# Performance work log

Hardware: AMD Instinct MI355X
Metric: run time of the kernel (lower is better)

## Reference

```python
import jax, jax.numpy as jnp
import numpy as np
from jax import lax

B, S, F, H, O, U = 512, 168, 12, 128, 3, 256
PERIODS = (3, 6, 12, 24)


def _glorot(key, shape):
    fan_in = shape[-1]
    fan_out = shape[-2] if len(shape) >= 2 else shape[-1]
    scale = jnp.sqrt(2.0 / (fan_in + fan_out))
    return jax.random.normal(key, shape, jnp.float32) * scale


def setup_inputs() -> dict:
    key = jax.random.key(0)
    ks = iter(jax.random.split(key, 64))
    inp = {"x": jax.random.normal(next(ks), (B, 1, F, S), jnp.float32)}
    # 3 SFF groups (group1: enc_in=12, groups 2/3: enc_in=3) share conv/linear shapes per period
    for p in PERIODS:
        k = 1 + 2 * (p // 2)
        inp[f"conv{p}"] = _glorot(next(ks), (3, k))             # [group, kernel]
        inp[f"lin{p}"] = _glorot(next(ks), (3, S // p, S // p))  # [group, seg_y, seg_x]
    inp["Wb0"] = _glorot(next(ks), (U, F + H)); inp["bb0"] = jnp.zeros((U,), jnp.float32)
    inp["Wb1"] = _glorot(next(ks), (U, U));     inp["bb1"] = jnp.zeros((U,), jnp.float32)
    inp["Wff1"] = _glorot(next(ks), (H, U));    inp["bff1"] = jnp.zeros((H,), jnp.float32)
    inp["Wff2"] = _glorot(next(ks), (H, U));    inp["bff2"] = jnp.zeros((H,), jnp.float32)
    inp["Wta"] = _glorot(next(ks), (H, U));     inp["bta"] = jnp.zeros((H,), jnp.float32)
    inp["Wtb"] = _glorot(next(ks), (H, U));     inp["btb"] = jnp.zeros((H,), jnp.float32)
    inp["Wfc"] = _glorot(next(ks), (O, H));     inp["bfc"] = jnp.zeros((O,), jnp.float32)
    inp["Wfits"] = _glorot(next(ks), (O, S, S))  # FF: individual per-channel linear seq->pred
    return inp


def _sff(x, conv_w, lin_w, p):
    # x: [B, S, C]; conv_w: [k]; lin_w: [seg_y, seg_x]
    Bx, Sx, C = x.shape
    xp = jnp.transpose(x, (0, 2, 1))                      # [B, C, S]
    xr = xp.reshape(Bx * C, 1, Sx)
    pad = p // 2
    conv = lax.conv_general_dilated(xr, conv_w.reshape(1, 1, -1), (1,), [(pad, pad)],
                                    dimension_numbers=("NCH", "OIH", "NCH"))
    xc = conv.reshape(Bx, C, Sx) + xp                     # residual smoothing
    seg = Sx // p
    xc = jnp.transpose(xc.reshape(Bx * C, seg, p), (0, 2, 1))  # [B*C, p, seg_x]
    y = jnp.einsum("npk,qk->npq", xc, lin_w)              # [B*C, p, seg_y]
    y = jnp.transpose(y, (0, 2, 1)).reshape(Bx, C, -1)    # [B, C, pred]
    return jnp.transpose(y, (0, 2, 1))                    # [B, pred, C]


def reference(x, conv3, lin3, conv6, lin6, conv12, lin12, conv24, lin24,
              Wb0, bb0, Wb1, bb1, Wff1, bff1, Wff2, bff2,
              Wta, bta, Wtb, btb, Wfc, bfc, Wfits):
    convs = {3: conv3, 6: conv6, 12: conv12, 24: conv24}
    lins = {3: lin3, 6: lin6, 12: lin12, 24: lin24}

    xs = jnp.transpose(x[:, 0], (0, 2, 1))                # [B, S, F]
    seq_mean = jnp.mean(xs, axis=1, keepdims=True)        # [B, 1, F]
    xs = xs - seq_mean

    x1 = sum(_sff(xs, convs[p][0], lins[p][0], p) for p in PERIODS) * 0.25   # [B,S,F]
    xin3 = x1[:, :, :3]
    x2 = sum(_sff(xin3, convs[p][1], lins[p][1], p) for p in PERIODS) * 0.25  # [B,S,3]
    x3 = sum(_sff(xin3, convs[p][2], lins[p][2], p) for p in PERIODS) * 0.25  # [B,S,3]

    # CfC recurrence (ts == 1.0 everywhere; dropout in eval mode = identity)
    def step(h, xt):
        z = jnp.concatenate([xt, h], axis=1)
        z = jax.nn.silu(z @ Wb0.T + bb0)
        z = jax.nn.silu(z @ Wb1.T + bb1)
        ff1 = jnp.tanh(z @ Wff1.T + bff1)
        ff2 = jnp.tanh(z @ Wff2.T + bff2)
        t_interp = jax.nn.sigmoid((z @ Wta.T + bta) + (z @ Wtb.T + btb))
        h_new = ff1 * (1.0 - t_interp) + t_interp * ff2
        return h_new, h_new

    h0 = jnp.zeros((x1.shape[0], Wff1.shape[0]), x1.dtype)
    _, hs = lax.scan(step, h0, jnp.transpose(x1, (1, 0, 2)))  # hs: [S, B, H]

    readout = jnp.einsum("sbh,oh->bso", hs, Wfc) + bfc        # [B, S, O]
    readout = readout + x3
    readout = jnp.einsum("bsc,cps->bpc", readout, Wfits)      # FF (per-channel S -> pred)
    return readout + seq_mean[:, :, :3] + x2
```

## Files before the change

kernel.cpp:

```cpp
#include <hip/hip_runtime.h>

#define BB 512
#define SS 168
#define FF 12
#define HH 128
#define UU 256

typedef unsigned short u16;
typedef unsigned int   u32;
typedef _Float16 f16x8 __attribute__((ext_vector_type(8)));
typedef float    f32x4 __attribute__((ext_vector_type(4)));

__device__ __forceinline__ float sigmoidf_(float x){ return __fdividef(1.f, 1.f + __expf(-x)); }
__device__ __forceinline__ float siluf_(float x){ return x * sigmoidf_(x); }
__device__ __forceinline__ float tanhf_(float x){
    float t = __expf(-2.f * fabsf(x));
    float y = __fdividef(1.f - t, 1.f + t);
    return copysignf(y, x);
}
__device__ __forceinline__ u16 f2h_(float v){ return __builtin_bit_cast(u16, (_Float16)v); }
__device__ __forceinline__ f16x8 bc8_(uint4 v){ return __builtin_bit_cast(f16x8, v); }
__device__ __forceinline__ int aslot_(int row, int k){
    return (k >> 5) * 512 + ((k & 31) >> 3) * 128 + row * 8 + (k & 7);
}

#define MFMA16(a, b, acc) __builtin_amdgcn_mfma_f32_16x16x32_f16((a), (b), (acc), 0, 0, 0)

#define PREP_BLOCKS 810
#define SFFA_BLOCKS (BB * FF)

__global__ __launch_bounds__(256) void front_kernel(
    const float* __restrict__ x,
    const float* __restrict__ c3,  const float* __restrict__ l3,
    const float* __restrict__ c6,  const float* __restrict__ l6,
    const float* __restrict__ c12, const float* __restrict__ l12,
    const float* __restrict__ c24, const float* __restrict__ l24,
    const float* __restrict__ Wb0, const float* __restrict__ Wb1,
    const float* __restrict__ Wff1, const float* __restrict__ Wff2,
    const float* __restrict__ Wta, const float* __restrict__ Wtb,
    const float* __restrict__ Wfc,
    u16* __restrict__ W0f, u16* __restrict__ W1f, u16* __restrict__ W4f,
    float* __restrict__ meanbuf, float* __restrict__ x1,
    float* __restrict__ x2, float* __restrict__ x3)
{
    if (blockIdx.x < PREP_BLOCKS) {
        int t = blockIdx.x * 256 + threadIdx.x;
        if (t < 43520) {
            int e = t & 7, c = (t >> 3) & 15, g = (t >> 7) & 3, rest = t >> 9;
            int s = rest % 5, tt = rest / 5;
            int k = s * 32 + g * 8 + e;
            float v;
            if (tt < 16) { int u = tt * 16 + c; v = (k < 140) ? Wb0[u * 140 + k] : 0.f; }
            else         { v = (c < 3 && k >= 12 && k < 140) ? Wfc[c * 128 + (k - 12)] : 0.f; }
            W0f[t] = f2h_(v);
        } else if (t < 43520 + 65536) {
            int t1 = t - 43520;
            int e = t1 & 7, c = (t1 >> 3) & 15, g = (t1 >> 7) & 3, rest = t1 >> 9;
            int s = rest & 7, tt = rest >> 3;
            int u = tt * 16 + c, k = s * 32 + g * 8 + e;
            W1f[t1] = f2h_(Wb1[u * 256 + k]);
        } else if (t < 43520 + 65536 + 98304) {
            int t2 = t - 109056;
            int e = t2 & 7, c = (t2 >> 3) & 15, g = (t2 >> 7) & 3, rest = t2 >> 9;
            int s = rest & 7, tt = rest >> 3;
            int u = (tt & 7) * 16 + c, k = s * 32 + g * 8 + e;
            float v;
            if      (tt < 8)  v = Wff1[u * 256 + k];
            else if (tt < 16) v = Wff2[u * 256 + k];
            else              v = Wta[u * 256 + k] + Wtb[u * 256 + k];
            W4f[t2] = f2h_(v);
        }
        return;
    }

    int bc = blockIdx.x - PREP_BLOCKS;
    int b = bc / FF, c = bc % FF;
    __shared__ float v[SS], cv[SS], red[256];
    int tid = threadIdx.x;

    float raw = 0.f;
    if (tid < SS) raw = x[(b * FF + c) * SS + tid];
    red[tid] = raw;
    __syncthreads();
    for (int off = 128; off > 0; off >>= 1) {
        if (tid < off) red[tid] += red[tid + off];
        __syncthreads();
    }
    float mv = red[0] * (1.f / SS);
    if (tid == 0) meanbuf[b * FF + c] = mv;
    if (tid < SS) v[tid] = raw - mv;
    __syncthreads();

    const float* cw[4]  = {c3, c6, c12, c24};
    const float* lwv[4] = {l3, l6, l12, l24};
    const int P[4] = {3, 6, 12, 24};
    float acc = 0.f;
    for (int pi = 0; pi < 4; ++pi) {
        int p = P[pi], pad = p >> 1, k = 1 + 2 * pad, seg = SS / p;
        const float* cwp = cw[pi];
        float cc = 0.f;
        if (tid < SS) {
            cc = v[tid];
            for (int j = 0; j < k; ++j) {
                int t = tid + j - pad;
                if (t >= 0 && t < SS) cc += cwp[j] * v[t];
            }
        }
        __syncthreads();
        if (tid < SS) cv[tid] = cc;
        __syncthreads();
        if (tid < SS) {
            int q = tid / p, ph = tid - q * p;
            const float* lwp = lwv[pi];
            float a = 0.f;
            for (int kk = 0; kk < seg; ++kk) a += lwp[q * seg + kk] * cv[kk * p + ph];
            acc += a;
        }
    }
    float x1v = 0.25f * acc;
    if (tid < SS) x1[(b * SS + tid) * FF + c] = x1v;
    if (c >= 3) return;

    __syncthreads();
    if (tid < SS) v[tid] = x1v;
    __syncthreads();
    float acc2 = 0.f, acc3 = 0.f;
    for (int pi = 0; pi < 4; ++pi) {
        int p = P[pi], pad = p >> 1, k = 1 + 2 * pad, seg = SS / p;
        for (int row = 1; row <= 2; ++row) {
            const float* cwp = cw[pi] + row * k;
            float cc = 0.f;
            if (tid < SS) {
                cc = v[tid];
                for (int j = 0; j < k; ++j) {
                    int t = tid + j - pad;
                    if (t >= 0 && t < SS) cc += cwp[j] * v[t];
                }
            }
            __syncthreads();
            if (tid < SS) cv[tid] = cc;
            __syncthreads();
            if (tid < SS) {
                int q = tid / p, ph = tid - q * p;
                const float* lwp = lwv[pi] + row * seg * seg;
                float a = 0.f;
                for (int kk = 0; kk < seg; ++kk) a += lwp[q * seg + kk] * cv[kk * p + ph];
                if (row == 1) acc2 += a; else acc3 += a;
            }
        }
    }
    if (tid < SS) {
        x2[(b * SS + tid) * 3 + c] = 0.25f * acc2;
        x3[(b * SS + tid) * 3 + c] = 0.25f * acc3;
    }
}

__global__ __launch_bounds__(512, 2) void scan_kernel(
    const float* __restrict__ x1g,
    const uint4* __restrict__ W0f, const uint4* __restrict__ W1f, const uint4* __restrict__ W4f,
    const float* __restrict__ bb0, const float* __restrict__ bb1,
    const float* __restrict__ bff1, const float* __restrict__ bff2,
    const float* __restrict__ bta,  const float* __restrict__ btb,
    const float* __restrict__ bfc,
    float* __restrict__ r1g)
{
    const int b0 = blockIdx.x * 4;
    const int tid = threadIdx.x;
    const int w = tid >> 6, lane = tid & 63;
    const int cl = lane & 15, grp = lane >> 4;

    __shared__ __align__(16) u16 W0ro_s[2560];
    __shared__ __align__(16) u16 xh[8064];
    __shared__ __align__(16) u16 zin_s[2560];
    __shared__ __align__(16) u16 z1_s[4096];
    __shared__ __align__(16) u16 z2_s[4096];
    __shared__ __align__(16) float r1s[2016];
    __shared__ float bfcs[4];

    uint4* W0ro4 = (uint4*)W0ro_s;
    uint4* zin4  = (uint4*)zin_s;
    uint4* z1_4  = (uint4*)z1_s;
    uint4* z2_4  = (uint4*)z2_s;

    f16x8 w0a[5], w0b[5];
    f16x8 w1f0[8], w1f1[8], w4a[8], w4b[8], w4c[8];
    #pragma unroll
    for (int s = 0; s < 5; ++s) {
        w0a[s] = bc8_(W0f[((w    ) * 5 + s) * 64 + lane]);
        w0b[s] = bc8_(W0f[((w + 8) * 5 + s) * 64 + lane]);
    }
    #pragma unroll
    for (int s = 0; s < 8; ++s) {
        w1f0[s] = bc8_(W1f[((w     ) * 8 + s) * 64 + lane]);
        w1f1[s] = bc8_(W1f[((w +  8) * 8 + s) * 64 + lane]);
        w4a[s]  = bc8_(W4f[((w     ) * 8 + s) * 64 + lane]);
        w4b[s]  = bc8_(W4f[((w +  8) * 8 + s) * 64 + lane]);
        w4c[s]  = bc8_(W4f[((w + 16) * 8 + s) * 64 + lane]);
    }
    const int u = w * 16 + cl;
    const float bz1a = bb0[u],  bz1b = bb0[128 + u];
    const float bz2a = bb1[u],  bz2b = bb1[128 + u];
    const float bf1r = bff1[u], bf2r = bff2[u];
    const float btsr = bta[u] + btb[u];

    for (int i = tid; i < 320; i += 512) W0ro4[i] = W0f[5120 + i];
    for (int i = tid; i < 8064; i += 512) {
        int s = i / 48, rem = i - s * 48, r = rem / 12, ii = rem - r * 12;
        xh[i] = f2h_(x1g[((b0 + r) * SS + s) * FF + ii]);
    }
    for (int i = tid; i < 320; i += 512) zin4[i] = make_uint4(0, 0, 0, 0);
    for (int i = tid; i < 512; i += 512) z1_4[i] = make_uint4(0, 0, 0, 0);
    for (int i = tid; i < 512; i += 512) z2_4[i] = make_uint4(0, 0, 0, 0);
    if (tid < 3) bfcs[tid] = bfc[tid];
    __syncthreads();
    if (tid < 48) {
        int r = tid / 12, i = tid % 12;
        zin_s[aslot_(r * 4, i)] = xh[tid];
    }
    __syncthreads();

    #pragma unroll 1
    for (int s = 0; s < SS; ++s) {
        f32x4 a1a0 = {0.f,0.f,0.f,0.f}, a1a1 = {0.f,0.f,0.f,0.f};
        f32x4 a1b0 = {0.f,0.f,0.f,0.f}, a1b1 = {0.f,0.f,0.f,0.f};
        f32x4 accr = {0.f,0.f,0.f,0.f};
        #pragma unroll
        for (int ks = 0; ks < 5; ++ks) {
            f16x8 av = bc8_(zin4[ks * 64 + lane]);
            if (ks & 1) { a1a1 = MFMA16(av, w0a[ks], a1a1); a1b1 = MFMA16(av, w0b[ks], a1b1); }
            else        { a1a0 = MFMA16(av, w0a[ks], a1a0); a1b0 = MFMA16(av, w0b[ks], a1b0); }
            if (w == 0) accr = MFMA16(av, bc8_(W0ro4[ks * 64 + lane]), accr);
        }
        if (w == 0 && s > 0 && cl < 3)
            r1s[grp * 504 + (s - 1) * 3 + cl] = accr[0] + bfcs[cl];

        {
            int tr = grp * 4;
            z1_s[aslot_(tr, u)]       = f2h_(siluf_(a1a0[0] + a1a1[0] + bz1a));
            z1_s[aslot_(tr, 128 + u)] = f2h_(siluf_(a1b0[0] + a1b1[0] + bz1b));
        }
        __syncthreads();

        f32x4 a2a0 = {0.f,0.f,0.f,0.f}, a2a1 = {0.f,0.f,0.f,0.f};
        f32x4 a2b0 = {0.f,0.f,0.f,0.f}, a2b1 = {0.f,0.f,0.f,0.f};
        #pragma unroll
        for (int ks = 0; ks < 8; ++ks) {
            f16x8 av = bc8_(z1_4[ks * 64 + lane]);
            if (ks & 1) { a2a1 = MFMA16(av, w1f0[ks], a2a1); a2b1 = MFMA16(av, w1f1[ks], a2b1); }
            else        { a2a0 = MFMA16(av, w1f0[ks], a2a0); a2b0 = MFMA16(av, w1f1[ks], a2b0); }
        }
        {
            int tr = grp * 4;
            z2_s[aslot_(tr, u)]       = f2h_(siluf_(a2a0[0] + a2a1[0] + bz2a));
            z2_s[aslot_(tr, 128 + u)] = f2h_(siluf_(a2b0[0] + a2b1[0] + bz2b));
        }
        __syncthreads();

        f32x4 c3a0 = {0.f,0.f,0.f,0.f}, c3a1 = {0.f,0.f,0.f,0.f};
        f32x4 c3b0 = {0.f,0.f,0.f,0.f}, c3b1 = {0.f,0.f,0.f,0.f};
        f32x4 c3c0 = {0.f,0.f,0.f,0.f}, c3c1 = {0.f,0.f,0.f,0.f};
        #pragma unroll
        for (int ks = 0; ks < 8; ++ks) {
            f16x8 av = bc8_(z2_4[ks * 64 + lane]);
            if (ks & 1) {
                c3a1 = MFMA16(av, w4a[ks], c3a1);
                c3b1 = MFMA16(av, w4b[ks], c3b1);
                c3c1 = MFMA16(av, w4c[ks], c3c1);
            } else {
                c3a0 = MFMA16(av, w4a[ks], c3a0);
                c3b0 = MFMA16(av, w4b[ks], c3b0);
                c3c0 = MFMA16(av, w4c[ks], c3c0);
            }
        }

        {
            float ff1v = tanhf_(c3a0[0] + c3a1[0] + bf1r);
            float ff2v = tanhf_(c3b0[0] + c3b1[0] + bf2r);
            float tv   = sigmoidf_(c3c0[0] + c3c1[0] + btsr);
            float h    = ff1v + tv * (ff2v - ff1v);
            zin_s[aslot_(grp * 4, 12 + u)] = f2h_(h);
        }
        if (tid >= 448 && tid < 496 && s + 1 < SS) {
            int idx = tid - 448;
            int r = idx / 12, i = idx % 12;
            zin_s[aslot_(r * 4, i)] = xh[(s + 1) * 48 + idx];
        }
        __syncthreads();
    }

    if (w == 0) {
        f32x4 accr = {0.f, 0.f, 0.f, 0.f};
        #pragma unroll
        for (int ks = 0; ks < 5; ++ks)
            accr = MFMA16(bc8_(zin4[ks * 64 + lane]),
                          bc8_(W0ro4[ks * 64 + lane]), accr);
        if (cl < 3)
            r1s[grp * 504 + 167 * 3 + cl] = accr[0] + bfcs[cl];
    }
    __syncthreads();
    for (int idx = tid; idx < 2016; idx += 512) {
        int r = idx / 504, rem = idx - r * 504;
        r1g[(b0 + r) * 504 + rem] = r1s[r * 504 + rem];
    }
}

__global__ __launch_bounds__(256) void fits_kernel(
    const float* __restrict__ r1, const float* __restrict__ x3,
    const float* __restrict__ Wfits,
    const float* __restrict__ x2, const float* __restrict__ meanbuf,
    float* __restrict__ out)
{
    int bid = blockIdx.x;
    int bt = bid & 7;
    int rest = bid >> 3;
    int c = rest % 3;
    int pt = rest / 3;
    int b0 = bt * 64, p0 = pt * 28;
    __shared__ float rT[168][65];
    __shared__ float wT[28][168];
    int t = threadIdx.x;
    for (int idx = t; idx < 64 * 168; idx += 256) {
        int b = idx / 168, s = idx - b * 168;
        int gi = ((b0 + b) * 168 + s) * 3 + c;
        rT[s][b] = r1[gi] + x3[gi];
    }
    for (int idx = t; idx < 28 * 168; idx += 256) {
        int p = idx / 168, s = idx - p * 168;
        wT[p][s] = Wfits[(c * 168 + p0 + p) * 168 + s];
    }
    __syncthreads();
    int b = t & 63, pq = t >> 6;
    float acc[7] = {0, 0, 0, 0, 0, 0, 0};
    for (int s = 0; s < 168; ++s) {
        float v = rT[s][b];
        #pragma unroll
        for (int j = 0; j < 7; ++j) acc[j] += v * wT[pq * 7 + j][s];
    }
    float mb = meanbuf[(b0 + b) * 12 + c];
    #pragma unroll
    for (int j = 0; j < 7; ++j) {
        int p = p0 + pq * 7 + j;
        int gi = ((b0 + b) * 168 + p) * 3 + c;
        out[gi] = acc[j] + mb + x2[gi];
    }
}

extern "C" void kernel_launch(void* const* d_in, const int* in_sizes, int n_in,
                              void* d_out, int out_size, void* d_ws, size_t ws_size,
                              hipStream_t stream) {
    const float* x    = (const float*)d_in[0];
    const float* c3   = (const float*)d_in[1];
    const float* l3   = (const float*)d_in[2];
    const float* c6   = (const float*)d_in[3];
    const float* l6   = (const float*)d_in[4];
    const float* c12  = (const float*)d_in[5];
    const float* l12  = (const float*)d_in[6];
    const float* c24  = (const float*)d_in[7];
    const float* l24  = (const float*)d_in[8];
    const float* Wb0  = (const float*)d_in[9];
    const float* bb0  = (const float*)d_in[10];
    const float* Wb1  = (const float*)d_in[11];
    const float* bb1  = (const float*)d_in[12];
    const float* Wff1 = (const float*)d_in[13];
    const float* bff1 = (const float*)d_in[14];
    const float* Wff2 = (const float*)d_in[15];
    const float* bff2 = (const float*)d_in[16];
    const float* Wta  = (const float*)d_in[17];
    const float* bta  = (const float*)d_in[18];
    const float* Wtb  = (const float*)d_in[19];
    const float* btb  = (const float*)d_in[20];
    const float* Wfc  = (const float*)d_in[21];
    const float* bfc  = (const float*)d_in[22];
    const float* Wfits= (const float*)d_in[23];

    float* ws      = (float*)d_ws;
    float* meanbuf = ws;
    float* x1      = meanbuf + 6144;
    float* x2      = x1 + 1032192;
    float* x3      = x2 + 258048;
    float* r1      = x3 + 258048;
    u16*   W0f     = (u16*)(r1 + 258048);
    u16*   W1f     = W0f + 43520;
    u16*   W4f     = W1f + 65536;
    float* out     = (float*)d_out;

    front_kernel<<<PREP_BLOCKS + SFFA_BLOCKS, 256, 0, stream>>>(
        x, c3, l3, c6, l6, c12, l12, c24, l24,
        Wb0, Wb1, Wff1, Wff2, Wta, Wtb, Wfc,
        W0f, W1f, W4f, meanbuf, x1, x2, x3);
    scan_kernel<<<BB / 4, 512, 0, stream>>>(x1,
                                            (const uint4*)W0f, (const uint4*)W1f, (const uint4*)W4f,
                                            bb0, bb1, bff1, bff2, bta, btb, bfc, r1);
    fits_kernel<<<144, 256, 0, stream>>>(r1, x3, Wfits, x2, meanbuf, out);
}
```

Measured before the change: 342.2 us.

## Fuse SFF front end, CfC scan and FF readout into one kernel

Merges the three launches into a single per-4-batch kernel. Each block computes the mean, SFF smoothing, the scan, and the Wfits projection in shared memory, and loads fp32 weights directly into fp16 MFMA fragments, so there is no separate weight-prep pass and no global round-trips for x1/x2/x3/r1. The 12-wide input projection moves out of the MFMA into scalar FMAs precomputed one step ahead, the K loop drops from 5 to 4, biases are folded into accumulator init, and s_setprio is added around the MFMA blocks. The cost is that every block now does redundant weight conversion and serial SFF/readout work on only 128 blocks, with heavy LDS use.

```diff
diff --git a/kernel.cpp b/kernel.cpp
--- a/kernel.cpp
+++ b/kernel.cpp
@@ -7,7 +7,6 @@
 #define UU 256
 
 typedef unsigned short u16;
-typedef unsigned int   u32;
 typedef _Float16 f16x8 __attribute__((ext_vector_type(8)));
 typedef float    f32x4 __attribute__((ext_vector_type(4)));
 
@@ -23,242 +22,264 @@
 __device__ __forceinline__ int aslot_(int row, int k){
     return (k >> 5) * 512 + ((k & 31) >> 3) * 128 + row * 8 + (k & 7);
 }
+__device__ __forceinline__ f16x8 pack8_(const float* p){
+    float4 a = *(const float4*)p, b = *(const float4*)(p + 4);
+    f16x8 r;
+    r[0]=(_Float16)a.x; r[1]=(_Float16)a.y; r[2]=(_Float16)a.z; r[3]=(_Float16)a.w;
+    r[4]=(_Float16)b.x; r[5]=(_Float16)b.y; r[6]=(_Float16)b.z; r[7]=(_Float16)b.w;
+    return r;
+}
+__device__ __forceinline__ f16x8 pack8sum_(const float* p, const float* q){
+    float4 a = *(const float4*)p, b = *(const float4*)(p + 4);
+    float4 c = *(const float4*)q, d = *(const float4*)(q + 4);
+    f16x8 r;
+    r[0]=(_Float16)(a.x+c.x); r[1]=(_Float16)(a.y+c.y); r[2]=(_Float16)(a.z+c.z); r[3]=(_Float16)(a.w+c.w);
+    r[4]=(_Float16)(b.x+d.x); r[5]=(_Float16)(b.y+d.y); r[6]=(_Float16)(b.z+d.z); r[7]=(_Float16)(b.w+d.w);
+    return r;
+}
 
 #define MFMA16(a, b, acc) __builtin_amdgcn_mfma_f32_16x16x32_f16((a), (b), (acc), 0, 0, 0)
 
-#define PREP_BLOCKS 810
-#define SFFA_BLOCKS (BB * FF)
-
-__global__ __launch_bounds__(256) void front_kernel(
-    const float* __restrict__ x,
-    const float* __restrict__ c3,  const float* __restrict__ l3,
-    const float* __restrict__ c6,  const float* __restrict__ l6,
-    const float* __restrict__ c12, const float* __restrict__ l12,
-    const float* __restrict__ c24, const float* __restrict__ l24,
-    const float* __restrict__ Wb0, const float* __restrict__ Wb1,
-    const float* __restrict__ Wff1, const float* __restrict__ Wff2,
-    const float* __restrict__ Wta, const float* __restrict__ Wtb,
-    const float* __restrict__ Wfc,
-    u16* __restrict__ W0f, u16* __restrict__ W1f, u16* __restrict__ W4f,
-    float* __restrict__ meanbuf, float* __restrict__ x1,
-    float* __restrict__ x2, float* __restrict__ x3)
-{
-    if (blockIdx.x < PREP_BLOCKS) {
-        int t = blockIdx.x * 256 + threadIdx.x;
-        if (t < 43520) {
-            int e = t & 7, c = (t >> 3) & 15, g = (t >> 7) & 3, rest = t >> 9;
-            int s = rest % 5, tt = rest / 5;
-            int k = s * 32 + g * 8 + e;
-            float v;
-            if (tt < 16) { int u = tt * 16 + c; v = (k < 140) ? Wb0[u * 140 + k] : 0.f; }
-            else         { v = (c < 3 && k >= 12 && k < 140) ? Wfc[c * 128 + (k - 12)] : 0.f; }
-            W0f[t] = f2h_(v);
-        } else if (t < 43520 + 65536) {
-            int t1 = t - 43520;
-            int e = t1 & 7, c = (t1 >> 3) & 15, g = (t1 >> 7) & 3, rest = t1 >> 9;
-            int s = rest & 7, tt = rest >> 3;
-            int u = tt * 16 + c, k = s * 32 + g * 8 + e;
-            W1f[t1] = f2h_(Wb1[u * 256 + k]);
-        } else if (t < 43520 + 65536 + 98304) {
-            int t2 = t - 109056;
-            int e = t2 & 7, c = (t2 >> 3) & 15, g = (t2 >> 7) & 3, rest = t2 >> 9;
-            int s = rest & 7, tt = rest >> 3;
-            int u = (tt & 7) * 16 + c, k = s * 32 + g * 8 + e;
-            float v;
-            if      (tt < 8)  v = Wff1[u * 256 + k];
-            else if (tt < 16) v = Wff2[u * 256 + k];
-            else              v = Wta[u * 256 + k] + Wtb[u * 256 + k];
-            W4f[t2] = f2h_(v);
-        }
-        return;
-    }
-
-    int bc = blockIdx.x - PREP_BLOCKS;
-    int b = bc / FF, c = bc % FF;
-    __shared__ float v[SS], cv[SS], red[256];
-    int tid = threadIdx.x;
-
-    float raw = 0.f;
-    if (tid < SS) raw = x[(b * FF + c) * SS + tid];
-    red[tid] = raw;
-    __syncthreads();
-    for (int off = 128; off > 0; off >>= 1) {
-        if (tid < off) red[tid] += red[tid + off];
-        __syncthreads();
-    }
-    float mv = red[0] * (1.f / SS);
-    if (tid == 0) meanbuf[b * FF + c] = mv;
-    if (tid < SS) v[tid] = raw - mv;
-    __syncthreads();
-
-    const float* cw[4]  = {c3, c6, c12, c24};
-    const float* lwv[4] = {l3, l6, l12, l24};
-    const int P[4] = {3, 6, 12, 24};
-    float acc = 0.f;
-    for (int pi = 0; pi < 4; ++pi) {
-        int p = P[pi], pad = p >> 1, k = 1 + 2 * pad, seg = SS / p;
-        const float* cwp = cw[pi];
-        float cc = 0.f;
-        if (tid < SS) {
-            cc = v[tid];
-            for (int j = 0; j < k; ++j) {
-                int t = tid + j - pad;
-                if (t >= 0 && t < SS) cc += cwp[j] * v[t];
-            }
-        }
-        __syncthreads();
-        if (tid < SS) cv[tid] = cc;
-        __syncthreads();
-        if (tid < SS) {
-            int q = tid / p, ph = tid - q * p;
-            const float* lwp = lwv[pi];
-            float a = 0.f;
-            for (int kk = 0; kk < seg; ++kk) a += lwp[q * seg + kk] * cv[kk * p + ph];
-            acc += a;
-        }
-    }
-    float x1v = 0.25f * acc;
-    if (tid < SS) x1[(b * SS + tid) * FF + c] = x1v;
-    if (c >= 3) return;
-
-    __syncthreads();
-    if (tid < SS) v[tid] = x1v;
-    __syncthreads();
-    float acc2 = 0.f, acc3 = 0.f;
-    for (int pi = 0; pi < 4; ++pi) {
-        int p = P[pi], pad = p >> 1, k = 1 + 2 * pad, seg = SS / p;
-        for (int row = 1; row <= 2; ++row) {
-            const float* cwp = cw[pi] + row * k;
-            float cc = 0.f;
-            if (tid < SS) {
-                cc = v[tid];
-                for (int j = 0; j < k; ++j) {
-                    int t = tid + j - pad;
-                    if (t >= 0 && t < SS) cc += cwp[j] * v[t];
-                }
-            }
-            __syncthreads();
-            if (tid < SS) cv[tid] = cc;
-            __syncthreads();
-            if (tid < SS) {
-                int q = tid / p, ph = tid - q * p;
-                const float* lwp = lwv[pi] + row * seg * seg;
-                float a = 0.f;
-                for (int kk = 0; kk < seg; ++kk) a += lwp[q * seg + kk] * cv[kk * p + ph];
-                if (row == 1) acc2 += a; else acc3 += a;
-            }
-        }
-    }
-    if (tid < SS) {
-        x2[(b * SS + tid) * 3 + c] = 0.25f * acc2;
-        x3[(b * SS + tid) * 3 + c] = 0.25f * acc3;
-    }
-}
-
-__global__ __launch_bounds__(512, 2) void scan_kernel(
-    const float* __restrict__ x1g,
-    const uint4* __restrict__ W0f, const uint4* __restrict__ W1f, const uint4* __restrict__ W4f,
-    const float* __restrict__ bb0, const float* __restrict__ bb1,
-    const float* __restrict__ bff1, const float* __restrict__ bff2,
-    const float* __restrict__ bta,  const float* __restrict__ btb,
-    const float* __restrict__ bfc,
-    float* __restrict__ r1g)
+__global__ __launch_bounds__(512, 2) void fused_kernel(
+    const float* __restrict__ xg,
+    const float* __restrict__ c3w,  const float* __restrict__ l3w,
+    const float* __restrict__ c6w,  const float* __restrict__ l6w,
+    const float* __restrict__ c12w, const float* __restrict__ l12w,
+    const float* __restrict__ c24w, const float* __restrict__ l24w,
+    const float* __restrict__ Wb0,  const float* __restrict__ bb0,
+    const float* __restrict__ Wb1,  const float* __restrict__ bb1,
+    const float* __restrict__ Wff1, const float* __restrict__ bff1,
+    const float* __restrict__ Wff2, const float* __restrict__ bff2,
+    const float* __restrict__ Wta,  const float* __restrict__ bta,
+    const float* __restrict__ Wtb,  const float* __restrict__ btb,
+    const float* __restrict__ Wfc,  const float* __restrict__ bfc,
+    const float* __restrict__ Wfits,
+    float* __restrict__ outg)
 {
     const int b0 = blockIdx.x * 4;
     const int tid = threadIdx.x;
     const int w = tid >> 6, lane = tid & 63;
     const int cl = lane & 15, grp = lane >> 4;
 
-    __shared__ __align__(16) u16 W0ro_s[2560];
-    __shared__ __align__(16) u16 xh[8064];
-    __shared__ __align__(16) u16 zin_s[2560];
-    __shared__ __align__(16) u16 z1_s[4096];
-    __shared__ __align__(16) u16 z2_s[4096];
-    __shared__ __align__(16) float r1s[2016];
+    __shared__ __align__(16) float xf[8064];
+    __shared__ __align__(16) float xraw[8064];
+    __shared__ __align__(16) float cvbuf[8064];
+    __shared__ __align__(16) float aux[6048];
+    __shared__ float meanloc[48];
     __shared__ float bfcs[4];
 
-    uint4* W0ro4 = (uint4*)W0ro_s;
+    u16* zin_s  = (u16*)xraw;
+    u16* z1_s   = ((u16*)xraw) + 2048;
+    u16* z2_s   = ((u16*)xraw) + 6144;
+    u16* W0ro_s = ((u16*)xraw) + 10240;
     uint4* zin4  = (uint4*)zin_s;
     uint4* z1_4  = (uint4*)z1_s;
     uint4* z2_4  = (uint4*)z2_s;
-
-    f16x8 w0a[5], w0b[5];
-    f16x8 w1f0[8], w1f1[8], w4a[8], w4b[8], w4c[8];
+    uint4* W0ro4 = (uint4*)W0ro_s;
+    float* r1s   = aux;
+    float* x2loc = aux + 2016;
+    float* x3loc = aux + 4032;
+
+    for (int i = tid; i < 8064; i += 512) {
+        int r = i / 2016, rem = i - r * 2016;
+        xraw[i] = xg[(b0 + r) * 2016 + rem];
+    }
+    if (tid < 3) bfcs[tid] = bfc[tid];
+    __syncthreads();
+
+    if (w < 6) {
+        int sidx = w * 8 + (lane >> 3), j = lane & 7;
+        float sum = 0.f;
+        for (int t = j; t < SS; t += 8) sum += xraw[sidx * 168 + t];
+        sum += __shfl_xor(sum, 1); sum += __shfl_xor(sum, 2); sum += __shfl_xor(sum, 4);
+        if (j == 0) meanloc[sidx] = sum * (1.f / 168.f);
+    }
+    __syncthreads();
+    for (int i = tid; i < 8064; i += 512) xraw[i] -= meanloc[i / 168];
+    __syncthreads();
+
+    const float* cws[4] = {c3w, c6w, c12w, c24w};
+    const float* lws[4] = {l3w, l6w, l12w, l24w};
+    const int    Pp[4]  = {3, 6, 12, 24};
+
+    float accA[16];
     #pragma unroll
-    for (int s = 0; s < 5; ++s) {
-        w0a[s] = bc8_(W0f[((w    ) * 5 + s) * 64 + lane]);
-        w0b[s] = bc8_(W0f[((w + 8) * 5 + s) * 64 + lane]);
-    }
+    for (int ii = 0; ii < 16; ++ii) accA[ii] = 0.f;
+    for (int pi = 0; pi < 4; ++pi) {
+        int p = Pp[pi], pad = p >> 1, kk_ = 1 + 2 * pad, seg = SS / p;
+        const float* cwp = cws[pi];
+        #pragma unroll 1
+        for (int ii = 0; ii < 16; ++ii) {
+            int i = tid + ii * 512;
+            if (i < 8064) {
+                int sr = i / 168, t = i - sr * 168;
+                const float* vs = &xraw[sr * 168];
+                float cc = vs[t];
+                for (int j = 0; j < kk_; ++j) {
+                    int tt = t + j - pad;
+                    if (tt >= 0 && tt < SS) cc += cwp[j] * vs[tt];
+                }
+                cvbuf[i] = cc;
+            }
+        }
+        __syncthreads();
+        const float* lwp = lws[pi];
+        #pragma unroll 1
+        for (int ii = 0; ii < 16; ++ii) {
+            int i = tid + ii * 512;
+            if (i < 8064) {
+                int sr = i / 168, t = i - sr * 168;
+                int q = t / p, ph = t - q * p;
+                const float* cvs = &cvbuf[sr * 168];
+                float a = 0.f;
+                for (int kk = 0; kk < seg; ++kk) a += lwp[q * seg + kk] * cvs[kk * p + ph];
+                accA[ii] += a;
+            }
+        }
+        __syncthreads();
+    }
+    #pragma unroll 1
+    for (int ii = 0; ii < 16; ++ii) {
+        int i = tid + ii * 512;
+        if (i < 8064) {
+            int sr = i / 168, t = i - sr * 168;
+            int r = sr / 12, c = sr - r * 12;
+            xf[r * 2016 + t * 12 + c] = 0.25f * accA[ii];
+        }
+    }
+    __syncthreads();
+
+    for (int i = tid; i < 256; i += 512) zin4[i] = make_uint4(0, 0, 0, 0);
+    for (int i = tid; i < 2048; i += 512) {
+        int ks = i >> 9, rem = i & 511;
+        int g = rem >> 7, c = (rem >> 3) & 15, e = rem & 7;
+        int k = ks * 32 + g * 8 + e;
+        W0ro_s[i] = f2h_((c < 3) ? Wfc[c * 128 + k] : 0.f);
+    }
+
+    float acc2[4], acc3[4];
     #pragma unroll
-    for (int s = 0; s < 8; ++s) {
-        w1f0[s] = bc8_(W1f[((w     ) * 8 + s) * 64 + lane]);
-        w1f1[s] = bc8_(W1f[((w +  8) * 8 + s) * 64 + lane]);
-        w4a[s]  = bc8_(W4f[((w     ) * 8 + s) * 64 + lane]);
-        w4b[s]  = bc8_(W4f[((w +  8) * 8 + s) * 64 + lane]);
-        w4c[s]  = bc8_(W4f[((w + 16) * 8 + s) * 64 + lane]);
-    }
+    for (int ii = 0; ii < 4; ++ii) { acc2[ii] = 0.f; acc3[ii] = 0.f; }
+    for (int pi = 0; pi < 4; ++pi) {
+        int p = Pp[pi], pad = p >> 1, kk_ = 1 + 2 * pad, seg = SS / p;
+        for (int row = 1; row <= 2; ++row) {
+            const float* cwp = cws[pi] + row * kk_;
+            #pragma unroll 1
+            for (int ii = 0; ii < 4; ++ii) {
+                int i = tid + ii * 512;
+                if (i < 2016) {
+                    int sr = i / 168, t = i - sr * 168;
+                    int r = sr / 3, c = sr - (sr / 3) * 3;
+                    float cc = xf[r * 2016 + t * 12 + c];
+                    for (int j = 0; j < kk_; ++j) {
+                        int tt = t + j - pad;
+                        if (tt >= 0 && tt < SS) cc += cwp[j] * xf[r * 2016 + tt * 12 + c];
+                    }
+                    cvbuf[i] = cc;
+                }
+            }
+            __syncthreads();
+            const float* lwp = lws[pi] + row * seg * seg;
+            #pragma unroll 1
+            for (int ii = 0; ii < 4; ++ii) {
+                int i = tid + ii * 512;
+                if (i < 2016) {
+                    int sr = i / 168, t = i - sr * 168;
+                    int q = t / p, ph = t - q * p;
+                    float a = 0.f;
+                    for (int kk = 0; kk < seg; ++kk) a += lwp[q * seg + kk] * cvbuf[sr * 168 + kk * p + ph];
+                    if (row == 1) acc2[ii] += a; else acc3[ii] += a;
+                }
+            }
+            __syncthreads();
+        }
+    }
+    #pragma unroll 1
+    for (int ii = 0; ii < 4; ++ii) {
+        int i = tid + ii * 512;
+        if (i < 2016) {
+            int sr = i / 168, t = i - sr * 168;
+            int r = sr / 3, c = sr - (sr / 3) * 3;
+            x2loc[r * 504 + t * 3 + c] = 0.25f * acc2[ii];
+            x3loc[r * 504 + t * 3 + c] = 0.25f * acc3[ii];
+        }
+    }
+
     const int u = w * 16 + cl;
+    f16x8 w0a[4], w0b[4], w1f0[8], w1f1[8], w4a[8], w4b[8], w4c[8];
+    #pragma unroll
+    for (int s8 = 0; s8 < 4; ++s8) {
+        int k0 = s8 * 32 + grp * 8;
+        w0a[s8] = pack8_(&Wb0[u * 140 + 12 + k0]);
+        w0b[s8] = pack8_(&Wb0[(128 + u) * 140 + 12 + k0]);
+    }
+    #pragma unroll
+    for (int s8 = 0; s8 < 8; ++s8) {
+        int k0 = s8 * 32 + grp * 8;
+        w1f0[s8] = pack8_(&Wb1[u * 256 + k0]);
+        w1f1[s8] = pack8_(&Wb1[(128 + u) * 256 + k0]);
+        w4a[s8]  = pack8_(&Wff1[u * 256 + k0]);
+        w4b[s8]  = pack8_(&Wff2[u * 256 + k0]);
+        w4c[s8]  = pack8sum_(&Wta[u * 256 + k0], &Wtb[u * 256 + k0]);
+    }
+    float w0xa[12], w0xb[12];
+    {
+        const float* pa = &Wb0[u * 140];
+        const float* pb = &Wb0[(128 + u) * 140];
+        #pragma unroll
+        for (int i = 0; i < 12; ++i) { w0xa[i] = pa[i]; w0xb[i] = pb[i]; }
+    }
     const float bz1a = bb0[u],  bz1b = bb0[128 + u];
     const float bz2a = bb1[u],  bz2b = bb1[128 + u];
     const float bf1r = bff1[u], bf2r = bff2[u];
     const float btsr = bta[u] + btb[u];
-
-    for (int i = tid; i < 320; i += 512) W0ro4[i] = W0f[5120 + i];
-    for (int i = tid; i < 8064; i += 512) {
-        int s = i / 48, rem = i - s * 48, r = rem / 12, ii = rem - r * 12;
-        xh[i] = f2h_(x1g[((b0 + r) * SS + s) * FF + ii]);
-    }
-    for (int i = tid; i < 320; i += 512) zin4[i] = make_uint4(0, 0, 0, 0);
-    for (int i = tid; i < 512; i += 512) z1_4[i] = make_uint4(0, 0, 0, 0);
-    for (int i = tid; i < 512; i += 512) z2_4[i] = make_uint4(0, 0, 0, 0);
-    if (tid < 3) bfcs[tid] = bfc[tid];
-    __syncthreads();
-    if (tid < 48) {
-        int r = tid / 12, i = tid % 12;
-        zin_s[aslot_(r * 4, i)] = xh[tid];
-    }
-    __syncthreads();
+    __syncthreads();
+
+    float z1xa = 0.f, z1xb = 0.f;
+    {
+        const float* xrow = &xf[grp * 2016];
+        #pragma unroll
+        for (int i = 0; i < 12; ++i) { float xv = xrow[i]; z1xa += w0xa[i] * xv; z1xb += w0xb[i] * xv; }
+    }
 
     #pragma unroll 1
     for (int s = 0; s < SS; ++s) {
-        f32x4 a1a0 = {0.f,0.f,0.f,0.f}, a1a1 = {0.f,0.f,0.f,0.f};
-        f32x4 a1b0 = {0.f,0.f,0.f,0.f}, a1b1 = {0.f,0.f,0.f,0.f};
-        f32x4 accr = {0.f,0.f,0.f,0.f};
-        #pragma unroll
-        for (int ks = 0; ks < 5; ++ks) {
+        f32x4 a1a0 = {z1xa + bz1a, 0.f, 0.f, 0.f}, a1a1 = {0.f, 0.f, 0.f, 0.f};
+        f32x4 a1b0 = {z1xb + bz1b, 0.f, 0.f, 0.f}, a1b1 = {0.f, 0.f, 0.f, 0.f};
+        f32x4 accr = {0.f, 0.f, 0.f, 0.f};
+        __builtin_amdgcn_s_setprio(1);
+        #pragma unroll
+        for (int ks = 0; ks < 4; ++ks) {
             f16x8 av = bc8_(zin4[ks * 64 + lane]);
             if (ks & 1) { a1a1 = MFMA16(av, w0a[ks], a1a1); a1b1 = MFMA16(av, w0b[ks], a1b1); }
             else        { a1a0 = MFMA16(av, w0a[ks], a1a0); a1b0 = MFMA16(av, w0b[ks], a1b0); }
             if (w == 0) accr = MFMA16(av, bc8_(W0ro4[ks * 64 + lane]), accr);
         }
+        __builtin_amdgcn_s_setprio(0);
         if (w == 0 && s > 0 && cl < 3)
             r1s[grp * 504 + (s - 1) * 3 + cl] = accr[0] + bfcs[cl];
-
-        {
-            int tr = grp * 4;
-            z1_s[aslot_(tr, u)]       = f2h_(siluf_(a1a0[0] + a1a1[0] + bz1a));
-            z1_s[aslot_(tr, 128 + u)] = f2h_(siluf_(a1b0[0] + a1b1[0] + bz1b));
-        }
-        __syncthreads();
-
-        f32x4 a2a0 = {0.f,0.f,0.f,0.f}, a2a1 = {0.f,0.f,0.f,0.f};
-        f32x4 a2b0 = {0.f,0.f,0.f,0.f}, a2b1 = {0.f,0.f,0.f,0.f};
+        z1_s[aslot_(grp * 4, u)]       = f2h_(siluf_(a1a0[0] + a1a1[0]));
+        z1_s[aslot_(grp * 4, 128 + u)] = f2h_(siluf_(a1b0[0] + a1b1[0]));
+        __syncthreads();
+
+        f32x4 a2a0 = {bz2a, 0.f, 0.f, 0.f}, a2a1 = {0.f, 0.f, 0.f, 0.f};
+        f32x4 a2b0 = {bz2b, 0.f, 0.f, 0.f}, a2b1 = {0.f, 0.f, 0.f, 0.f};
+        __builtin_amdgcn_s_setprio(1);
         #pragma unroll
         for (int ks = 0; ks < 8; ++ks) {
             f16x8 av = bc8_(z1_4[ks * 64 + lane]);
             if (ks & 1) { a2a1 = MFMA16(av, w1f0[ks], a2a1); a2b1 = MFMA16(av, w1f1[ks], a2b1); }
             else        { a2a0 = MFMA16(av, w1f0[ks], a2a0); a2b0 = MFMA16(av, w1f1[ks], a2b0); }
         }
-        {
-            int tr = grp * 4;
-            z2_s[aslot_(tr, u)]       = f2h_(siluf_(a2a0[0] + a2a1[0] + bz2a));
-            z2_s[aslot_(tr, 128 + u)] = f2h_(siluf_(a2b0[0] + a2b1[0] + bz2b));
-        }
-        __syncthreads();
-
-        f32x4 c3a0 = {0.f,0.f,0.f,0.f}, c3a1 = {0.f,0.f,0.f,0.f};
-        f32x4 c3b0 = {0.f,0.f,0.f,0.f}, c3b1 = {0.f,0.f,0.f,0.f};
-        f32x4 c3c0 = {0.f,0.f,0.f,0.f}, c3c1 = {0.f,0.f,0.f,0.f};
+        __builtin_amdgcn_s_setprio(0);
+        z2_s[aslot_(grp * 4, u)]       = f2h_(siluf_(a2a0[0] + a2a1[0]));
+        z2_s[aslot_(grp * 4, 128 + u)] = f2h_(siluf_(a2b0[0] + a2b1[0]));
+        __syncthreads();
+
+        f32x4 c3a0 = {bf1r, 0.f, 0.f, 0.f}, c3a1 = {0.f, 0.f, 0.f, 0.f};
+        f32x4 c3b0 = {bf2r, 0.f, 0.f, 0.f}, c3b1 = {0.f, 0.f, 0.f, 0.f};
+        f32x4 c3c0 = {btsr, 0.f, 0.f, 0.f}, c3c1 = {0.f, 0.f, 0.f, 0.f};
+        __builtin_amdgcn_s_setprio(1);
         #pragma unroll
         for (int ks = 0; ks < 8; ++ks) {
             f16x8 av = bc8_(z2_4[ks * 64 + lane]);
@@ -272,18 +293,23 @@
                 c3c0 = MFMA16(av, w4c[ks], c3c0);
             }
         }
+        __builtin_amdgcn_s_setprio(0);
 
         {
-            float ff1v = tanhf_(c3a0[0] + c3a1[0] + bf1r);
-            float ff2v = tanhf_(c3b0[0] + c3b1[0] + bf2r);
-            float tv   = sigmoidf_(c3c0[0] + c3c1[0] + btsr);
+            int sn = (s + 1 < SS) ? s + 1 : s;
+            const float* xrow = &xf[grp * 2016 + sn * 12];
+            float za = 0.f, zb = 0.f;
+            #pragma unroll
+            for (int i = 0; i < 12; ++i) { float xv = xrow[i]; za += w0xa[i] * xv; zb += w0xb[i] * xv; }
+            z1xa = za; z1xb = zb;
+        }
+
+        {
+            float ff1v = tanhf_(c3a0[0] + c3a1[0]);
+            float ff2v = tanhf_(c3b0[0] + c3b1[0]);
+            float tv   = sigmoidf_(c3c0[0] + c3c1[0]);
             float h    = ff1v + tv * (ff2v - ff1v);
-            zin_s[aslot_(grp * 4, 12 + u)] = f2h_(h);
-        }
-        if (tid >= 448 && tid < 496 && s + 1 < SS) {
-            int idx = tid - 448;
-            int r = idx / 12, i = idx % 12;
-            zin_s[aslot_(r * 4, i)] = xh[(s + 1) * 48 + idx];
+            zin_s[aslot_(grp * 4, u)] = f2h_(h);
         }
         __syncthreads();
     }
@@ -291,57 +317,33 @@
     if (w == 0) {
         f32x4 accr = {0.f, 0.f, 0.f, 0.f};
         #pragma unroll
-        for (int ks = 0; ks < 5; ++ks)
-            accr = MFMA16(bc8_(zin4[ks * 64 + lane]),
-                          bc8_(W0ro4[ks * 64 + lane]), accr);
-        if (cl < 3)
-            r1s[grp * 504 + 167 * 3 + cl] = accr[0] + bfcs[cl];
-    }
-    __syncthreads();
-    for (int idx = tid; idx < 2016; idx += 512) {
-        int r = idx / 504, rem = idx - r * 504;
-        r1g[(b0 + r) * 504 + rem] = r1s[r * 504 + rem];
-    }
-}
-
-__global__ __launch_bounds__(256) void fits_kernel(
-    const float* __restrict__ r1, const float* __restrict__ x3,
-    const float* __restrict__ Wfits,
-    const float* __restrict__ x2, const float* __restrict__ meanbuf,
-    float* __restrict__ out)
-{
-    int bid = blockIdx.x;
-    int bt = bid & 7;
-    int rest = bid >> 3;
-    int c = rest % 3;
-    int pt = rest / 3;
-    int b0 = bt * 64, p0 = pt * 28;
-    __shared__ float rT[168][65];
-    __shared__ float wT[28][168];
-    int t = threadIdx.x;
-    for (int idx = t; idx < 64 * 168; idx += 256) {
-        int b = idx / 168, s = idx - b * 168;
-        int gi = ((b0 + b) * 168 + s) * 3 + c;
-        rT[s][b] = r1[gi] + x3[gi];
-    }
-    for (int idx = t; idx < 28 * 168; idx += 256) {
-        int p = idx / 168, s = idx - p * 168;
-        wT[p][s] = Wfits[(c * 168 + p0 + p) * 168 + s];
-    }
-    __syncthreads();
-    int b = t & 63, pq = t >> 6;
-    float acc[7] = {0, 0, 0, 0, 0, 0, 0};
-    for (int s = 0; s < 168; ++s) {
-        float v = rT[s][b];
-        #pragma unroll
-        for (int j = 0; j < 7; ++j) acc[j] += v * wT[pq * 7 + j][s];
-    }
-    float mb = meanbuf[(b0 + b) * 12 + c];
-    #pragma unroll
-    for (int j = 0; j < 7; ++j) {
-        int p = p0 + pq * 7 + j;
-        int gi = ((b0 + b) * 168 + p) * 3 + c;
-        out[gi] = acc[j] + mb + x2[gi];
+        for (int ks = 0; ks < 4; ++ks)
+            accr = MFMA16(bc8_(zin4[ks * 64 + lane]), bc8_(W0ro4[ks * 64 + lane]), accr);
+        if (cl < 3) r1s[grp * 504 + 167 * 3 + cl] = accr[0] + bfcs[cl];
+    }
+    __syncthreads();
+    for (int i = tid; i < 2016; i += 512) r1s[i] += x3loc[i];
+    __syncthreads();
+    {
+        int r = tid >> 7, idx = tid & 127;
+        if (idx < 126) {
+            const float* rrow = &r1s[r * 504];
+            #pragma unroll
+            for (int j = 0; j < 4; ++j) {
+                int o = idx * 4 + j;
+                int p = o / 3, c = o - p * 3;
+                const float* wrow = &Wfits[(c * 168 + p) * 168];
+                float acc = 0.f;
+                for (int s4 = 0; s4 < 42; ++s4) {
+                    float4 wv = *(const float4*)&wrow[s4 * 4];
+                    acc += rrow[(s4 * 4 + 0) * 3 + c] * wv.x
+                         + rrow[(s4 * 4 + 1) * 3 + c] * wv.y
+                         + rrow[(s4 * 4 + 2) * 3 + c] * wv.z
+                         + rrow[(s4 * 4 + 3) * 3 + c] * wv.w;
+                }
+                outg[(b0 + r) * 504 + o] = acc + meanloc[r * 12 + c] + x2loc[r * 504 + o];
+            }
+        }
     }
 }
 
@@ -372,24 +374,10 @@
     const float* Wfc  = (const float*)d_in[21];
     const float* bfc  = (const float*)d_in[22];
     const float* Wfits= (const float*)d_in[23];
-
-    float* ws      = (float*)d_ws;
-    float* meanbuf = ws;
-    float* x1      = meanbuf + 6144;
-    float* x2      = x1 + 1032192;
-    float* x3      = x2 + 258048;
-    float* r1      = x3 + 258048;
-    u16*   W0f     = (u16*)(r1 + 258048);
-    u16*   W1f     = W0f + 43520;
-    u16*   W4f     = W1f + 65536;
-    float* out     = (float*)d_out;
-
-    front_kernel<<<PREP_BLOCKS + SFFA_BLOCKS, 256, 0, stream>>>(
+    float* out = (float*)d_out;
+
+    fused_kernel<<<BB / 4, 512, 0, stream>>>(
         x, c3, l3, c6, l6, c12, l12, c24, l24,
-        Wb0, Wb1, Wff1, Wff2, Wta, Wtb, Wfc,
-        W0f, W1f, W4f, meanbuf, x1, x2, x3);
-    scan_kernel<<<BB / 4, 512, 0, stream>>>(x1,
-                                            (const uint4*)W0f, (const uint4*)W1f, (const uint4*)W4f,
-                                            bb0, bb1, bff1, bff2, bta, btb, bfc, r1);
-    fits_kernel<<<144, 256, 0, stream>>>(r1, x3, Wfits, x2, meanbuf, out);
-}
+        Wb0, bb0, Wb1, bb1, Wff1, bff1, Wff2, bff2,
+        Wta, bta, Wtb, btb, Wfc, bfc, Wfits, out);
+}
```

Measured after the change: 664.5 us. 1.94x slower.
